# Performance work log

Hardware: AMD Instinct MI355X
Metric: run time of the kernel (lower is better)

Reference implementation:

```python
import jax, jax.numpy as jnp
import numpy as np
from jax import lax


def _conv2d(x, w, b, stride):
    # x: [B,C,H,W], w: [O,I,kh,kw], b: [O]
    y = lax.conv_general_dilated(
        x, w, window_strides=(stride, stride), padding='VALID',
        dimension_numbers=('NCHW', 'OIHW', 'NCHW'))
    return y + b[None, :, None, None]


def setup_inputs() -> dict:
    key = jax.random.key(0)
    ks = jax.random.split(key, 4)
    B, C, H, W = 8, 128, 128, 128
    x = jax.random.normal(ks[0], (B, C, H, W), dtype=jnp.float32)
    # conv weights, scaled like torch default init (~1/sqrt(fan_in))
    Wq = jax.random.normal(ks[1], (C, C, 2, 2), dtype=jnp.float32) / np.sqrt(C * 4)
    Wk = jax.random.normal(ks[2], (C, C, 2, 2), dtype=jnp.float32) / np.sqrt(C * 4)
    Wv = jax.random.normal(ks[3], (C, C, 1, 1), dtype=jnp.float32) / np.sqrt(C)
    bq = jnp.zeros((C,), dtype=jnp.float32)
    bk = jnp.zeros((C,), dtype=jnp.float32)
    bv = jnp.zeros((C,), dtype=jnp.float32)
    return {'x': x, 'Wq': Wq, 'bq': bq, 'Wk': Wk, 'bk': bk, 'Wv': Wv, 'bv': bv}


def reference(x, Wq, bq, Wk, bk, Wv, bv):
    B, C, H, W = x.shape
    # query/key: 2x2 stride-2 convs -> [B, C, (H//2)*(W//2)]
    q = _conv2d(x, Wq, bq, 2).reshape(B, C, -1)
    k = _conv2d(x, Wk, bk, 2).reshape(B, C, -1)
    # value: 1x1 conv -> [B, C, H*W]
    v = _conv2d(x, Wv, bv, 1).reshape(B, C, -1)
    # energy: [B, C, C]
    energy = jnp.einsum('bcn,bdn->bcd', q, k)
    # max-subtract trick: softmax over (row_max - energy)
    energy_new = jnp.max(energy, axis=-1, keepdims=True) - energy
    attention = jax.nn.softmax(energy_new, axis=-1)
    out = jnp.einsum('bcd,bdn->bcn', attention, v)
    return out.reshape(B, C, H, W)
```

## Files before the change

### kernel.cpp

```cpp
#include <hip/hip_runtime.h>
#include <math.h>


typedef float f32x4 __attribute__((ext_vector_type(4)));
typedef short s16x8 __attribute__((ext_vector_type(8)));

__device__ __forceinline__ unsigned short f2bf(float f) {
  union { __bf16 b; unsigned short u; } v;
  v.b = (__bf16)f;
  return v.u;
}
__device__ __forceinline__ float bf2f(unsigned short h) {
  union { unsigned u; float f; } v; v.u = ((unsigned)h) << 16;
  return v.f;
}
__device__ __forceinline__ unsigned pack2(unsigned short a, unsigned short b) {
  return (unsigned)a | ((unsigned)b << 16);
}

__global__ __launch_bounds__(256) void k_prep(
    const float* __restrict__ Wq, const float* __restrict__ Wk,
    unsigned short* __restrict__ Wth, unsigned short* __restrict__ Wtl) {
  const int f = (blockIdx.x * 256 + threadIdx.x) * 4;
  const int row = f >> 9;
  const int k   = f & 511;
  const float* src = (row < 128) ? &Wq[row * 512 + k] : &Wk[(row - 128) * 512 + k];
  float4 v = *(const float4*)src;
  unsigned short h0 = f2bf(v.x), h1 = f2bf(v.y), h2 = f2bf(v.z), h3 = f2bf(v.w);
  unsigned short l0 = f2bf(v.x - bf2f(h0)), l1 = f2bf(v.y - bf2f(h1));
  unsigned short l2 = f2bf(v.z - bf2f(h2)), l3 = f2bf(v.w - bf2f(h3));
  const int di = (k >> 5) * 8192 + row * 32 + (k & 31);
  *(ushort4*)&Wth[di] = make_ushort4(h0, h1, h2, h3);
  *(ushort4*)&Wtl[di] = make_ushort4(l0, l1, l2, l3);
}

__global__ __launch_bounds__(256, 3) void k_conv_energy(
    const float* __restrict__ x,
    const unsigned short* __restrict__ Wth, const unsigned short* __restrict__ Wtl,
    const float* __restrict__ bq, const float* __restrict__ bk,
    float* __restrict__ epart) {
  __shared__ unsigned short LDS[16384];
  unsigned short* Th = LDS;
  unsigned short* Tl = LDS + 8192;

  const int t = threadIdx.x;
  const int nt = blockIdx.x, b = blockIdx.y;
  const int w = t >> 6, lane = t & 63;
  const int lrow = lane & 15, lkb = lane >> 4;

  const int pp = t >> 4;
  const int ci_l = pp >> 1, kh = pp & 1;
  const int i16 = t & 15;
  const int klb = ci_l * 4 + kh * 2;
  const float* xb = x + ((size_t)b << 21);
  const float* xrow = xb + (size_t)ci_l * 16384 + (2 * nt + kh) * 128 + 2 * i16;

  f32x4 acc[4][4];
#pragma unroll
  for (int m = 0; m < 4; ++m)
#pragma unroll
    for (int n = 0; n < 4; ++n) acc[m][n] = (f32x4){0.f, 0.f, 0.f, 0.f};

  s16x8 pfh[4], pfl[4];
  float2 pv[2][4];
  const int aoff = (w * 64 + lrow) * 32 + lkb * 8;

#pragma unroll
  for (int m = 0; m < 4; ++m) {
    pfh[m] = *(const s16x8*)&Wth[aoff + m * 512];
    pfl[m] = *(const s16x8*)&Wtl[aoff + m * 512];
  }
  {
    float2 v0 = *(const float2*)&xrow[0];
    float2 v1 = *(const float2*)&xrow[32];
    float2 v2 = *(const float2*)&xrow[64];
    float2 v3 = *(const float2*)&xrow[96];
    unsigned short hx, hy;
    hx = f2bf(v0.x); hy = f2bf(v0.y);
    *(unsigned*)&LDS[(i16     ) * 40 + klb] = pack2(hx, hy);
    *(unsigned*)&LDS[2560 + (i16     ) * 40 + klb] = pack2(f2bf(v0.x - bf2f(hx)), f2bf(v0.y - bf2f(hy)));
    hx = f2bf(v1.x); hy = f2bf(v1.y);
    *(unsigned*)&LDS[(i16 + 16) * 40 + klb] = pack2(hx, hy);
    *(unsigned*)&LDS[2560 + (i16 + 16) * 40 + klb] = pack2(f2bf(v1.x - bf2f(hx)), f2bf(v1.y - bf2f(hy)));
    hx = f2bf(v2.x); hy = f2bf(v2.y);
    *(unsigned*)&LDS[(i16 + 32) * 40 + klb] = pack2(hx, hy);
    *(unsigned*)&LDS[2560 + (i16 + 32) * 40 + klb] = pack2(f2bf(v2.x - bf2f(hx)), f2bf(v2.y - bf2f(hy)));
    hx = f2bf(v3.x); hy = f2bf(v3.y);
    *(unsigned*)&LDS[(i16 + 48) * 40 + klb] = pack2(hx, hy);
    *(unsigned*)&LDS[2560 + (i16 + 48) * 40 + klb] = pack2(f2bf(v3.x - bf2f(hx)), f2bf(v3.y - bf2f(hy)));
  }
#pragma unroll
  for (int g = 0; g < 4; ++g)
    pv[1][g] = *(const float2*)&xrow[(size_t)8 * 16384 + 32 * g];
  __syncthreads();

#pragma unroll
  for (int step = 0; step < 16; ++step) {
    const int cur = step & 1;
    const unsigned short* Bh = LDS + cur * 5120;
    const unsigned short* Bl = Bh + 2560;
    s16x8 bfh[4], bfl[4];
#pragma unroll
    for (int nf = 0; nf < 4; ++nf) {
      const int bidx = (nf * 16 + lrow) * 40 + lkb * 8;
      bfh[nf] = *(const s16x8*)&Bh[bidx];
      bfl[nf] = *(const s16x8*)&Bl[bidx];
    }
#pragma unroll
    for (int m = 0; m < 4; ++m)
#pragma unroll
      for (int n = 0; n < 4; ++n) {
        acc[m][n] = __builtin_amdgcn_mfma_f32_16x16x32_bf16(pfh[m], bfh[n], acc[m][n], 0, 0, 0);
        acc[m][n] = __builtin_amdgcn_mfma_f32_16x16x32_bf16(pfh[m], bfl[n], acc[m][n], 0, 0, 0);
        acc[m][n] = __builtin_amdgcn_mfma_f32_16x16x32_bf16(pfl[m], bfh[n], acc[m][n], 0, 0, 0);
      }
    if (step < 15) {
      const unsigned short* Wh_n = Wth + (step + 1) * 8192;
      const unsigned short* Wl_n = Wtl + (step + 1) * 8192;
#pragma unroll
      for (int m = 0; m < 4; ++m) {
        pfh[m] = *(const s16x8*)&Wh_n[aoff + m * 512];
        pfl[m] = *(const s16x8*)&Wl_n[aoff + m * 512];
      }
    }
    if (step < 14) {
#pragma unroll
      for (int g = 0; g < 4; ++g)
        pv[cur][g] = *(const float2*)&xrow[(size_t)(step + 2) * 8 * 16384 + 32 * g];
    }
    if (step < 15) {
      unsigned short* Nh = LDS + (cur ^ 1) * 5120;
      unsigned short* Nl = Nh + 2560;
#pragma unroll
      for (int g = 0; g < 4; ++g) {
        const int n = i16 + 16 * g;
        unsigned short hx = f2bf(pv[cur ^ 1][g].x), hy = f2bf(pv[cur ^ 1][g].y);
        *(unsigned*)&Nh[n * 40 + klb] = pack2(hx, hy);
        *(unsigned*)&Nl[n * 40 + klb] = pack2(f2bf(pv[cur ^ 1][g].x - bf2f(hx)),
                                              f2bf(pv[cur ^ 1][g].y - bf2f(hy)));
      }
      asm volatile("s_waitcnt lgkmcnt(0)" ::: "memory");
      __builtin_amdgcn_s_barrier();
    }
  }
  __syncthreads();

  const float* biasp = (w < 2) ? bq : bk;
  const int rb = (w & 1) * 64;
  float biasr[16];
#pragma unroll
  for (int m = 0; m < 4; ++m)
#pragma unroll
    for (int i = 0; i < 4; ++i)
      biasr[m * 4 + i] = biasp[rb + m * 16 + (lane >> 4) * 4 + i];

  f32x4 e[4][4];
#pragma unroll
  for (int m = 0; m < 4; ++m)
#pragma unroll
    for (int n = 0; n < 4; ++n) e[m][n] = (f32x4){0.f, 0.f, 0.f, 0.f};

  const int mrow0 = (w >> 1) * 64;
  const int nrow0 = 128 + (w & 1) * 64;

#pragma unroll
  for (int ks = 0; ks < 2; ++ks) {
#pragma unroll
    for (int m = 0; m < 4; ++m) {
      const int r0 = w * 64 + m * 16 + (lane >> 4) * 4;
#pragma unroll
      for (int nn = 0; nn < 2; ++nn) {
        const int n = 2 * ks + nn;
        const int cl = nn * 16 + lrow;
        const int cl8 = cl >> 3, c7 = cl & 7;
#pragma unroll
        for (int i = 0; i < 4; ++i) {
          const int r = r0 + i;
          const float vv = acc[m][n][i] + biasr[m * 4 + i];
          const unsigned short h = f2bf(vv);
          const unsigned short l = f2bf(vv - bf2f(h));
          const int ad = r * 32 + ((cl8 ^ (r & 3)) << 3) + c7;
          Th[ad] = h;
          Tl[ad] = l;
        }
      }
    }
    __syncthreads();
    {
      s16x8 qh[4], ql[4], kh8[4], kl8[4];
#pragma unroll
      for (int m = 0; m < 4; ++m) {
        const int r = mrow0 + m * 16 + lrow;
        const int ad = r * 32 + ((lkb ^ (r & 3)) << 3);
        qh[m] = *(const s16x8*)&Th[ad];
        ql[m] = *(const s16x8*)&Tl[ad];
      }
#pragma unroll
      for (int n = 0; n < 4; ++n) {
        const int r = nrow0 + n * 16 + lrow;
        const int ad = r * 32 + ((lkb ^ (r & 3)) << 3);
        kh8[n] = *(const s16x8*)&Th[ad];
        kl8[n] = *(const s16x8*)&Tl[ad];
      }
#pragma unroll
      for (int m = 0; m < 4; ++m)
#pragma unroll
        for (int n = 0; n < 4; ++n) {
          e[m][n] = __builtin_amdgcn_mfma_f32_16x16x32_bf16(qh[m], kh8[n], e[m][n], 0, 0, 0);
          e[m][n] = __builtin_amdgcn_mfma_f32_16x16x32_bf16(qh[m], kl8[n], e[m][n], 0, 0, 0);
          e[m][n] = __builtin_amdgcn_mfma_f32_16x16x32_bf16(ql[m], kh8[n], e[m][n], 0, 0, 0);
        }
    }
    if (ks == 0) __syncthreads();
  }

  float* ep = epart + ((size_t)b * 64 + nt) * 16384;
#pragma unroll
  for (int m = 0; m < 4; ++m) {
    const int qr = (w >> 1) * 64 + m * 16 + (lane >> 4) * 4;
#pragma unroll
    for (int n = 0; n < 4; ++n) {
      const int kr = (w & 1) * 64 + n * 16 + lrow;
#pragma unroll
      for (int i = 0; i < 4; ++i) ep[(size_t)(qr + i) * 128 + kr] = e[m][n][i];
    }
  }
}

__global__ __launch_bounds__(256) void k_softmax_M(
    const float* __restrict__ epart, const float* __restrict__ Wv,
    const float* __restrict__ bv, float* __restrict__ Mbuf,
    float* __restrict__ outbb) {
  __shared__ float As[4][128];
  const int t = threadIdx.x;
  const int wid = t >> 6, lane = t & 63;
  const int b = blockIdx.x >> 5;
  const int c = (blockIdx.x & 31) * 4 + wid;
  const int d0 = lane * 2;

  float2 s = make_float2(0.f, 0.f);
#pragma unroll 4
  for (int p = 0; p < 64; ++p) {
    float2 e = *(const float2*)&epart[((size_t)b * 64 + p) * 16384 + c * 128 + d0];
    s.x += e.x; s.y += e.y;
  }
  float mn = fminf(s.x, s.y);
#pragma unroll
  for (int off = 1; off < 64; off <<= 1) mn = fminf(mn, __shfl_xor(mn, off));
  const float p0 = expf(mn - s.x);
  const float p1 = expf(mn - s.y);
  float tot = p0 + p1;
#pragma unroll
  for (int off = 1; off < 64; off <<= 1) tot += __shfl_xor(tot, off);
  const float inv = 1.f / tot;
  const float a0 = p0 * inv, a1 = p1 * inv;

  const float2 bvv = *(const float2*)&bv[d0];
  float ob = a0 * bvv.x + a1 * bvv.y;
#pragma unroll
  for (int off = 1; off < 64; off <<= 1) ob += __shfl_xor(ob, off);
  if (lane == 0) outbb[b * 128 + c] = ob;

  As[wid][d0] = a0;
  As[wid][d0 + 1] = a1;
  float m0 = 0.f, m1 = 0.f;
#pragma unroll 4
  for (int d = 0; d < 128; ++d) {
    const float a = As[wid][d];
    const float2 wv = *(const float2*)&Wv[d * 128 + d0];
    m0 = fmaf(a, wv.x, m0);
    m1 = fmaf(a, wv.y, m1);
  }
  *(float2*)&Mbuf[(size_t)b * 16384 + c * 128 + d0] = make_float2(m0, m1);
}

__global__ __launch_bounds__(256) void k_out(
    const float* __restrict__ x, const float* __restrict__ Mbuf,
    const float* __restrict__ outbb, float* __restrict__ out) {
  __shared__ unsigned short Ms[128 * 40];
  __shared__ unsigned short Xs[128 * 40];
  const int t = threadIdx.x;
  const int nt = blockIdx.x, b = blockIdx.y;
  const int wid = t >> 6, lane = t & 63;
  const int wr = wid >> 1, wc = wid & 1;
  const int lrow = lane & 15, lkb = lane >> 4;
  const int am = t >> 1, ak0 = (t & 1) * 16;
  const int xkl = (t >> 5) * 4;
  const int xc0 = (t & 31) * 4;

  const float* xb = x + ((size_t)b << 21);
  const float* Mb = Mbuf + (size_t)b * 16384;
  float* ob = out + ((size_t)b << 21);

  f32x4 acc[4][4];
#pragma unroll
  for (int m = 0; m < 4; ++m)
#pragma unroll
    for (int n = 0; n < 4; ++n) acc[m][n] = (f32x4){0.f, 0.f, 0.f, 0.f};

  for (int step = 0; step < 4; ++step) {
    const int kk = step * 32;
    {
      float w[16];
      *(float4*)&w[0]  = *(const float4*)&Mb[am * 128 + kk + ak0];
      *(float4*)&w[4]  = *(const float4*)&Mb[am * 128 + kk + ak0 + 4];
      *(float4*)&w[8]  = *(const float4*)&Mb[am * 128 + kk + ak0 + 8];
      *(float4*)&w[12] = *(const float4*)&Mb[am * 128 + kk + ak0 + 12];
      unsigned short hs[16];
#pragma unroll
      for (int i = 0; i < 16; ++i) hs[i] = f2bf(w[i]);
      *(uint4*)&Ms[am * 40 + ak0]     = *(uint4*)&hs[0];
      *(uint4*)&Ms[am * 40 + ak0 + 8] = *(uint4*)&hs[8];
    }
#pragma unroll
    for (int q = 0; q < 4; ++q) {
      const int kl = xkl + q;
      float4 v = *(const float4*)&xb[(size_t)(kk + kl) * 16384 + nt * 128 + xc0];
      Xs[(xc0 + 0) * 40 + kl] = f2bf(v.x);
      Xs[(xc0 + 1) * 40 + kl] = f2bf(v.y);
      Xs[(xc0 + 2) * 40 + kl] = f2bf(v.z);
      Xs[(xc0 + 3) * 40 + kl] = f2bf(v.w);
    }
    __syncthreads();
    s16x8 af[4], bf[4];
#pragma unroll
    for (int m = 0; m < 4; ++m)
      af[m] = *(const s16x8*)&Ms[(wr * 64 + m * 16 + lrow) * 40 + lkb * 8];
#pragma unroll
    for (int n = 0; n < 4; ++n)
      bf[n] = *(const s16x8*)&Xs[(wc * 64 + n * 16 + lrow) * 40 + lkb * 8];
#pragma unroll
    for (int m = 0; m < 4; ++m)
#pragma unroll
      for (int n = 0; n < 4; ++n)
        acc[m][n] = __builtin_amdgcn_mfma_f32_16x16x32_bf16(af[m], bf[n], acc[m][n], 0, 0, 0);
    __syncthreads();
  }
#pragma unroll
  for (int m = 0; m < 4; ++m) {
    const int r0 = wr * 64 + m * 16 + (lane >> 4) * 4;
#pragma unroll
    for (int n = 0; n < 4; ++n) {
      const int gc = nt * 128 + wc * 64 + n * 16 + (lane & 15);
#pragma unroll
      for (int i = 0; i < 4; ++i) {
        const int row = r0 + i;
        ob[(size_t)row * 16384 + gc] = acc[m][n][i] + outbb[b * 128 + row];
      }
    }
  }
}

extern "C" void kernel_launch(void* const* d_in, const int* in_sizes, int n_in,
                              void* d_out, int out_size, void* d_ws, size_t ws_size,
                              hipStream_t stream) {
  const float* x  = (const float*)d_in[0];
  const float* Wq = (const float*)d_in[1];
  const float* bq = (const float*)d_in[2];
  const float* Wk = (const float*)d_in[3];
  const float* bk = (const float*)d_in[4];
  const float* Wv = (const float*)d_in[5];
  const float* bv = (const float*)d_in[6];
  float* out = (float*)d_out;
  char* ws = (char*)d_ws;

  float* epart = (float*)ws;
  float* Mbuf  = (float*)(ws + 33554432);
  float* outbb = (float*)(ws + 34078720);
  unsigned short* Wth = (unsigned short*)(ws + 34082816);
  unsigned short* Wtl = (unsigned short*)(ws + 34344960);

  hipLaunchKernelGGL(k_prep, dim3(128), dim3(256), 0, stream, Wq, Wk, Wth, Wtl);
  hipLaunchKernelGGL(k_conv_energy, dim3(64, 8), dim3(256), 0, stream,
                     x, Wth, Wtl, bq, bk, epart);
  hipLaunchKernelGGL(k_softmax_M, dim3(256), dim3(256), 0, stream,
                     epart, Wv, bv, Mbuf, outbb);
  hipLaunchKernelGGL(k_out, dim3(128, 8), dim3(256), 0, stream,
                     x, Mbuf, outbb, out);
}
```

Before: 84.59 us.

## Store M pre-swizzled in bf16 and double-buffer x tiles in k_out

k_softmax_M now writes M directly as bf16 in a k-step-blocked layout that k_out can read straight into MFMA A-fragments from global memory, so the per-step fp32 load, convert and LDS staging of M goes away. k_out also double-buffers the x tile in LDS and prefetches the next tiles into registers while MFMAs run, replacing two barriers per step with one. The costs are higher register pressure from the prefetch buffers and uncoalesced-looking global fragment loads for M, which rely on L2 caching.

Result: faster. 81.10 us (median of 2 runs) (-4.1%).

```diff
diff --git a/kernel.cpp b/kernel.cpp
--- a/kernel.cpp
+++ b/kernel.cpp
@@ -229,7 +229,7 @@
 
 __global__ __launch_bounds__(256) void k_softmax_M(
     const float* __restrict__ epart, const float* __restrict__ Wv,
-    const float* __restrict__ bv, float* __restrict__ Mbuf,
+    const float* __restrict__ bv, unsigned short* __restrict__ Mt,
     float* __restrict__ outbb) {
   __shared__ float As[4][128];
   const int t = threadIdx.x;
@@ -271,25 +271,26 @@
     m0 = fmaf(a, wv.x, m0);
     m1 = fmaf(a, wv.y, m1);
   }
-  *(float2*)&Mbuf[(size_t)b * 16384 + c * 128 + d0] = make_float2(m0, m1);
+  const int sk = lane >> 4;
+  const int ko = (lane * 2) & 31;
+  *(unsigned*)&Mt[(size_t)b * 16384 + sk * 4096 + c * 32 + ko] =
+      pack2(f2bf(m0), f2bf(m1));
 }
 
 __global__ __launch_bounds__(256) void k_out(
-    const float* __restrict__ x, const float* __restrict__ Mbuf,
+    const float* __restrict__ x, const unsigned short* __restrict__ Mt,
     const float* __restrict__ outbb, float* __restrict__ out) {
-  __shared__ unsigned short Ms[128 * 40];
-  __shared__ unsigned short Xs[128 * 40];
+  __shared__ unsigned short Xs[10240];
   const int t = threadIdx.x;
   const int nt = blockIdx.x, b = blockIdx.y;
   const int wid = t >> 6, lane = t & 63;
   const int wr = wid >> 1, wc = wid & 1;
   const int lrow = lane & 15, lkb = lane >> 4;
-  const int am = t >> 1, ak0 = (t & 1) * 16;
   const int xkl = (t >> 5) * 4;
   const int xc0 = (t & 31) * 4;
 
   const float* xb = x + ((size_t)b << 21);
-  const float* Mb = Mbuf + (size_t)b * 16384;
+  const unsigned short* Mb = Mt + (size_t)b * 16384;
   float* ob = out + ((size_t)b << 21);
 
   f32x4 acc[4][4];
@@ -298,43 +299,54 @@
 #pragma unroll
     for (int n = 0; n < 4; ++n) acc[m][n] = (f32x4){0.f, 0.f, 0.f, 0.f};
 
+  float4 pv[2][4];
+#pragma unroll
+  for (int q = 0; q < 4; ++q) {
+    float4 v = *(const float4*)&xb[(size_t)(xkl + q) * 16384 + nt * 128 + xc0];
+    Xs[(xc0 + 0) * 40 + xkl + q] = f2bf(v.x);
+    Xs[(xc0 + 1) * 40 + xkl + q] = f2bf(v.y);
+    Xs[(xc0 + 2) * 40 + xkl + q] = f2bf(v.z);
+    Xs[(xc0 + 3) * 40 + xkl + q] = f2bf(v.w);
+  }
+#pragma unroll
+  for (int q = 0; q < 4; ++q)
+    pv[1][q] = *(const float4*)&xb[(size_t)(32 + xkl + q) * 16384 + nt * 128 + xc0];
+  __syncthreads();
+
+#pragma unroll
   for (int step = 0; step < 4; ++step) {
-    const int kk = step * 32;
-    {
-      float w[16];
-      *(float4*)&w[0]  = *(const float4*)&Mb[am * 128 + kk + ak0];
-      *(float4*)&w[4]  = *(const float4*)&Mb[am * 128 + kk + ak0 + 4];
-      *(float4*)&w[8]  = *(const float4*)&Mb[am * 128 + kk + ak0 + 8];
-      *(float4*)&w[12] = *(const float4*)&Mb[am * 128 + kk + ak0 + 12];
-      unsigned short hs[16];
-#pragma unroll
-      for (int i = 0; i < 16; ++i) hs[i] = f2bf(w[i]);
-      *(uint4*)&Ms[am * 40 + ak0]     = *(uint4*)&hs[0];
-      *(uint4*)&Ms[am * 40 + ak0 + 8] = *(uint4*)&hs[8];
-    }
-#pragma unroll
-    for (int q = 0; q < 4; ++q) {
-      const int kl = xkl + q;
-      float4 v = *(const float4*)&xb[(size_t)(kk + kl) * 16384 + nt * 128 + xc0];
-      Xs[(xc0 + 0) * 40 + kl] = f2bf(v.x);
-      Xs[(xc0 + 1) * 40 + kl] = f2bf(v.y);
-      Xs[(xc0 + 2) * 40 + kl] = f2bf(v.z);
-      Xs[(xc0 + 3) * 40 + kl] = f2bf(v.w);
-    }
-    __syncthreads();
-    s16x8 af[4], bf[4];
+    const int cur = step & 1;
+    const unsigned short* Bx = Xs + cur * 5120;
+    s16x8 bf[4];
+#pragma unroll
+    for (int n = 0; n < 4; ++n)
+      bf[n] = *(const s16x8*)&Bx[(wc * 64 + n * 16 + lrow) * 40 + lkb * 8];
+    s16x8 af[4];
 #pragma unroll
     for (int m = 0; m < 4; ++m)
-      af[m] = *(const s16x8*)&Ms[(wr * 64 + m * 16 + lrow) * 40 + lkb * 8];
-#pragma unroll
-    for (int n = 0; n < 4; ++n)
-      bf[n] = *(const s16x8*)&Xs[(wc * 64 + n * 16 + lrow) * 40 + lkb * 8];
+      af[m] = *(const s16x8*)&Mb[step * 4096 + (wr * 64 + m * 16 + lrow) * 32 + lkb * 8];
+    if (step < 2) {
+#pragma unroll
+      for (int q = 0; q < 4; ++q)
+        pv[cur][q] = *(const float4*)&xb[(size_t)((step + 2) * 32 + xkl + q) * 16384 + nt * 128 + xc0];
+    }
 #pragma unroll
     for (int m = 0; m < 4; ++m)
 #pragma unroll
       for (int n = 0; n < 4; ++n)
         acc[m][n] = __builtin_amdgcn_mfma_f32_16x16x32_bf16(af[m], bf[n], acc[m][n], 0, 0, 0);
-    __syncthreads();
+    if (step < 3) {
+      unsigned short* Nx = Xs + (cur ^ 1) * 5120;
+#pragma unroll
+      for (int q = 0; q < 4; ++q) {
+        Nx[(xc0 + 0) * 40 + xkl + q] = f2bf(pv[cur ^ 1][q].x);
+        Nx[(xc0 + 1) * 40 + xkl + q] = f2bf(pv[cur ^ 1][q].y);
+        Nx[(xc0 + 2) * 40 + xkl + q] = f2bf(pv[cur ^ 1][q].z);
+        Nx[(xc0 + 3) * 40 + xkl + q] = f2bf(pv[cur ^ 1][q].w);
+      }
+      asm volatile("s_waitcnt lgkmcnt(0)" ::: "memory");
+      __builtin_amdgcn_s_barrier();
+    }
   }
 #pragma unroll
   for (int m = 0; m < 4; ++m) {
@@ -365,16 +377,16 @@
   char* ws = (char*)d_ws;
 
   float* epart = (float*)ws;
-  float* Mbuf  = (float*)(ws + 33554432);
-  float* outbb = (float*)(ws + 34078720);
-  unsigned short* Wth = (unsigned short*)(ws + 34082816);
-  unsigned short* Wtl = (unsigned short*)(ws + 34344960);
+  unsigned short* Mt = (unsigned short*)(ws + 33554432);
+  float* outbb = (float*)(ws + 33816576);
+  unsigned short* Wth = (unsigned short*)(ws + 33820672);
+  unsigned short* Wtl = (unsigned short*)(ws + 34082816);
 
   hipLaunchKernelGGL(k_prep, dim3(128), dim3(256), 0, stream, Wq, Wk, Wth, Wtl);
   hipLaunchKernelGGL(k_conv_energy, dim3(64, 8), dim3(256), 0, stream,
                      x, Wth, Wtl, bq, bk, epart);
   hipLaunchKernelGGL(k_softmax_M, dim3(256), dim3(256), 0, stream,
-                     epart, Wv, bv, Mbuf, outbb);
+                     epart, Wv, bv, Mt, outbb);
   hipLaunchKernelGGL(k_out, dim3(128, 8), dim3(256), 0, stream,
-                     x, Mbuf, outbb, out);
-}
+                     x, Mt, outbb, out);
+}
```
